# Performance work log

Measured on AMD Instinct MI355X. Metric: run time of the kernel, lower is better.

## Reference

```python
import jax, jax.numpy as jnp
import numpy as np

EPS = 1e-5
DIM = 32          # head_dim
HEADS = 8         # in_channels // dim * heads_ratio = 256 // 32

def hardswish(x):
    return x * jnp.clip(x + 3.0, 0.0, 6.0) / 6.0

def conv1x1(x, w):
    # w: (C_out, C_in); x: (B, C_in, H, W)
    return jnp.einsum('oi,bihw->bohw', w, x)

def dwconv(x, w, pad):
    # depthwise conv, w: (C, 1, kh, kw)
    return jax.lax.conv_general_dilated(
        x, w, (1, 1), [(pad, pad), (pad, pad)],
        dimension_numbers=('NCHW', 'OIHW', 'NCHW'),
        feature_group_count=x.shape[1])

def gconv1x1(x, w, groups):
    # grouped 1x1 conv, w: (C_out, C_in//groups, 1, 1)
    return jax.lax.conv_general_dilated(
        x, w, (1, 1), [(0, 0), (0, 0)],
        dimension_numbers=('NCHW', 'OIHW', 'NCHW'),
        feature_group_count=groups)


def setup_inputs() -> dict:
    key = jax.random.key(0)
    ks = jax.random.split(key, 12)
    B, C, H, W = 16, 256, 32, 32
    td = HEADS * DIM          # 256 (total_dim per branch)
    c3 = 3 * td               # 768
    mid = 4 * C               # 1024 (expand_ratio=4)

    def rn(k, shape, fan_in):
        return jax.random.normal(k, shape, jnp.float32) * (1.0 / np.sqrt(fan_in))

    return {
        'x': jax.random.normal(ks[0], (B, C, H, W), jnp.float32),
        # LiteMLA
        'w_qkv': rn(ks[1], (c3, C), C),                 # 1x1, bias=False, no norm
        'w_agg_dw': rn(ks[2], (c3, 1, 5, 5), 25),       # depthwise 5x5, pad 2
        'w_agg_pw': rn(ks[3], (c3, DIM, 1, 1), DIM),    # grouped 1x1, groups=3*HEADS
        'w_proj': rn(ks[4], (C, 2 * td), 2 * td),       # 1x1, bias=False (BN follows)
        'bn_proj_scale': jnp.ones((C,), jnp.float32) + 0.1 * jax.random.normal(ks[5], (C,), jnp.float32),
        'bn_proj_bias': 0.1 * jax.random.normal(ks[6], (C,), jnp.float32),
        # MBConv
        'w_mb1': rn(ks[7], (mid, C), C),
        'b_mb1': jnp.zeros((mid,), jnp.float32),
        'w_mb_dw': rn(ks[8], (mid, 1, 3, 3), 9),
        'b_mb_dw': jnp.zeros((mid,), jnp.float32),
        'w_mb2': rn(ks[9], (C, mid), mid),              # bias=False (BN follows)
        'bn2_scale': jnp.ones((C,), jnp.float32) + 0.1 * jax.random.normal(ks[10], (C,), jnp.float32),
        'bn2_bias': 0.1 * jax.random.normal(ks[11], (C,), jnp.float32),
    }


def reference(x, w_qkv, w_agg_dw, w_agg_pw, w_proj, bn_proj_scale, bn_proj_bias,
              w_mb1, b_mb1, w_mb_dw, b_mb_dw, w_mb2, bn2_scale, bn2_bias):
    B, C, H, W = x.shape
    # ---- LiteMLA context module (residual) ----
    qkv = conv1x1(x, w_qkv)                                   # (B, 768, H, W)
    agg = gconv1x1(dwconv(qkv, w_agg_dw, 2), w_agg_pw, 3 * HEADS)
    ms = jnp.concatenate([qkv, agg], axis=1)                  # (B, 1536, H, W)
    nh = ms.shape[1] // (3 * DIM)                             # 16 total heads
    t = ms.reshape(B, nh, 3 * DIM, H * W).transpose(0, 1, 3, 2)  # (B, nh, HW, 3*DIM)
    q, k, v = jnp.split(t, 3, axis=-1)                        # each (B, nh, HW, DIM)
    q = jax.nn.relu(q).astype(jnp.float32)
    k = jax.nn.relu(k).astype(jnp.float32)
    v = jnp.pad(v.astype(jnp.float32), ((0, 0), (0, 0), (0, 0), (0, 1)),
                constant_values=1.0)                          # (B, nh, HW, DIM+1)
    kv = jnp.einsum('bhnd,bhne->bhde', k, v)                  # (B, nh, DIM, DIM+1)
    out = jnp.einsum('bhnd,bhde->bhne', q, kv)                # (B, nh, HW, DIM+1)
    out = out[..., :-1] / (out[..., -1:] + EPS)
    out = out.astype(x.dtype)
    out = out.transpose(0, 1, 3, 2).reshape(B, nh * DIM, H, W)  # (B, 512, H, W)
    out = conv1x1(out, w_proj)
    out = out * bn_proj_scale[:, None, None] + bn_proj_bias[:, None, None]
    x = x + out                                               # residual
    # ---- MBConv local module (residual) ----
    h = hardswish(conv1x1(x, w_mb1) + b_mb1[:, None, None])
    h = hardswish(dwconv(h, w_mb_dw, 1) + b_mb_dw[:, None, None])
    h = conv1x1(h, w_mb2)
    h = h * bn2_scale[:, None, None] + bn2_bias[:, None, None]
    return x + h
```

## Files before the change

kernel.cpp:

```cpp
#include <hip/hip_runtime.h>
#include <hip/hip_bf16.h>


typedef unsigned short u16;
typedef __attribute__((ext_vector_type(8))) short short8;
typedef __attribute__((ext_vector_type(4))) short short4v;
typedef __attribute__((ext_vector_type(4))) float f32x4;

#define HW 1024
#define EPSV 1e-5f
#define MFMA16(a, b, c) __builtin_amdgcn_mfma_f32_16x16x32_bf16((a), (b), (c), 0, 0, 0)

__device__ __forceinline__ u16 f2bf(float f) {
    union { __hip_bfloat16 h; u16 u; } c; c.h = __float2bfloat16(f); return c.u;
}
__device__ __forceinline__ float bf2f(u16 u) {
    union { u16 u; __hip_bfloat16 h; } c; c.u = u; return __bfloat162float(c.h);
}
__device__ __forceinline__ float hswish(float v) {
    return v * fminf(fmaxf(v + 3.f, 0.f), 6.f) * (1.f / 6.f);
}

__global__ __launch_bounds__(256) void prep_k(
    const float* __restrict__ x,  u16* __restrict__ xb,
    const float* __restrict__ wq, u16* __restrict__ wqb,
    const float* __restrict__ wp, u16* __restrict__ wpb,
    const float* __restrict__ w1, u16* __restrict__ w1b,
    const float* __restrict__ w2, u16* __restrict__ w2b)
{
    const int N0 = 4194304, N1 = 196608, N2 = 131072, N3 = 262144;
    const int total = N0 + N1 + N2 + N3 + 262144;
    for (int i = blockIdx.x * 256 + threadIdx.x; i < total; i += gridDim.x * 256) {
        int id = i;
        if (id < N0) { xb[id]  = f2bf(x[id]);  continue; } id -= N0;
        if (id < N1) { wqb[id] = f2bf(wq[id]); continue; } id -= N1;
        if (id < N2) { wpb[id] = f2bf(wp[id]); continue; } id -= N2;
        if (id < N3) { w1b[id] = f2bf(w1[id]); continue; } id -= N3;
        w2b[id] = f2bf(w2[id]);
    }
}

template<int EPI>
__global__ __launch_bounds__(256) void gemm_bf(
    const u16* __restrict__ A, const u16* __restrict__ Bact,
    const float* __restrict__ s1, const float* __restrict__ s2,
    const float* __restrict__ Rres, float* __restrict__ outF,
    u16* __restrict__ outB, int M, int K)
{
    const int b  = blockIdx.z;
    const int n0 = blockIdx.x * 128;
    const int m0 = blockIdx.y * 128;
    const int t  = threadIdx.x;
    const int lr = t & 15, lg = (t >> 4) & 3;
    const int wid = t >> 6, wm = wid >> 1, wn = wid & 1;

    __shared__ u16 As[128 * 64];
    __shared__ u16 Bs[128 * 64];

    const u16* Bp = Bact + (size_t)b * K * HW;

    f32x4 zero4 = {0.f, 0.f, 0.f, 0.f};
    f32x4 acc[4][4];
    #pragma unroll
    for (int i = 0; i < 4; ++i)
        #pragma unroll
        for (int j = 0; j < 4; ++j) acc[i][j] = zero4;

    for (int k0 = 0; k0 < K; k0 += 64) {
        {
            const u16* Ab = A + (size_t)m0 * K + k0;
            #pragma unroll
            for (int u = 0; u < 4; ++u) {
                int id = t + u * 256;
                int row = id >> 3, c = id & 7;
                short8 v = *(const short8*)(Ab + (size_t)row * K + c * 8);
                *(short8*)(&As[row * 64 + ((c ^ (row & 7)) * 8)]) = v;
            }
        }
        {
            const u16* Bb = Bp + (size_t)k0 * HW + n0;
            int n = t & 127, kh = t >> 7;
            #pragma unroll
            for (int u = 0; u < 4; ++u) {
                int c = kh * 4 + u;
                short8 v;
                #pragma unroll
                for (int g = 0; g < 8; ++g)
                    v[g] = (short)Bb[(size_t)(c * 8 + g) * HW + n];
                *(short8*)(&Bs[n * 64 + ((c ^ (n & 7)) * 8)]) = v;
            }
        }
        __syncthreads();
        #pragma unroll
        for (int kk = 0; kk < 2; ++kk) {
            short8 a[4], bb[4];
            #pragma unroll
            for (int i = 0; i < 4; ++i) {
                int row = wm * 64 + i * 16 + lr;
                a[i] = *(const short8*)(&As[row * 64 + (((kk * 4 + lg) ^ (lr & 7)) * 8)]);
            }
            #pragma unroll
            for (int j = 0; j < 4; ++j) {
                int row = wn * 64 + j * 16 + lr;
                bb[j] = *(const short8*)(&Bs[row * 64 + (((kk * 4 + lg) ^ (lr & 7)) * 8)]);
            }
            #pragma unroll
            for (int i = 0; i < 4; ++i)
                #pragma unroll
                for (int j = 0; j < 4; ++j)
                    acc[i][j] = MFMA16(a[i], bb[j], acc[i][j]);
        }
        __syncthreads();
    }

    const size_t obase = (size_t)b * M * HW;
    #pragma unroll
    for (int i = 0; i < 4; ++i) {
        #pragma unroll
        for (int r = 0; r < 4; ++r) {
            const int grow = m0 + wm * 64 + i * 16 + lg * 4 + r;
            float p1 = 0.f, p2 = 0.f;
            if (EPI == 1) { p1 = s1[grow]; }
            if (EPI >= 2) { p1 = s1[grow]; p2 = s2[grow]; }
            #pragma unroll
            for (int j = 0; j < 4; ++j) {
                const int gcol = n0 + wn * 64 + j * 16 + lr;
                const size_t off = obase + (size_t)grow * HW + gcol;
                float v = acc[i][j][r];
                if (EPI == 0) { outB[off] = f2bf(v); }
                if (EPI == 1) { v = hswish(v + p1); outB[off] = f2bf(v); }
                if (EPI == 2) { v = v * p1 + p2 + Rres[off]; outF[off] = v; outB[off] = f2bf(v); }
                if (EPI == 3) { v = v * p1 + p2 + Rres[off]; outF[off] = v; }
            }
        }
    }
}

template<int KS, int PAD, int NCH, bool HS>
__global__ __launch_bounds__(256) void dwconv_k(
    const u16* __restrict__ in, const float* __restrict__ w,
    const float* __restrict__ bias, u16* __restrict__ out)
{
    constexpr int T = 32 + 2 * PAD;
    __shared__ float tile[T * T];
    const int plane = blockIdx.x;
    const int c = plane % NCH;
    const u16* ip = in + (size_t)plane * HW;
    const int t = threadIdx.x;
    for (int idx = t; idx < T * T; idx += 256) {
        int r = idx / T, cc = idx % T;
        int gr = r - PAD, gc = cc - PAD;
        float v = 0.f;
        if ((unsigned)gr < 32u && (unsigned)gc < 32u) v = bf2f(ip[gr * 32 + gc]);
        tile[idx] = v;
    }
    float wl[KS * KS];
    #pragma unroll
    for (int u = 0; u < KS * KS; ++u) wl[u] = w[c * KS * KS + u];
    const float bv = HS ? bias[c] : 0.f;
    __syncthreads();
    #pragma unroll
    for (int pj = 0; pj < 4; ++pj) {
        const int px = t + pj * 256;
        const int pr = px >> 5, pc = px & 31;
        float s = bv;
        #pragma unroll
        for (int dr = 0; dr < KS; ++dr)
            #pragma unroll
            for (int dc = 0; dc < KS; ++dc)
                s += tile[(pr + dr) * T + pc + dc] * wl[dr * KS + dc];
        if (HS) s = hswish(s);
        out[(size_t)plane * HW + px] = f2bf(s);
    }
}

__global__ __launch_bounds__(256) void gconv_k(
    const u16* __restrict__ dw, const float* __restrict__ wpw,
    u16* __restrict__ agg)
{
    const int gx = blockIdx.x;
    const int g = gx >> 2, nt = gx & 3;
    const int b = blockIdx.y;
    const int n0 = nt * 256;
    const int t = threadIdx.x;
    __shared__ float dt[32][256];
    __shared__ float wl[32 * 32];
    const u16* dp = dw + ((size_t)b * 768 + g * 32) * HW + n0;
    for (int idx = t; idx < 32 * 256; idx += 256) {
        int i = idx >> 8, nn = idx & 255;
        dt[i][nn] = bf2f(dp[(size_t)i * HW + nn]);
    }
    for (int idx = t; idx < 1024; idx += 256) wl[idx] = wpw[g * 1024 + idx];
    __syncthreads();
    float acc[32] = {};
    #pragma unroll
    for (int i = 0; i < 32; ++i) {
        const float d = dt[i][t];
        #pragma unroll
        for (int oc = 0; oc < 32; ++oc) acc[oc] += wl[oc * 32 + i] * d;
    }
    u16* ap = agg + ((size_t)b * 768 + g * 32) * HW + n0;
    #pragma unroll
    for (int oc = 0; oc < 32; ++oc) ap[(size_t)oc * HW + t] = f2bf(acc[oc]);
}

__global__ __launch_bounds__(64) void kv_k(
    const u16* __restrict__ qkvb, const u16* __restrict__ aggb,
    float* __restrict__ kvp)
{
    const int blk = blockIdx.x;
    const int bh = blk >> 2, nc = blk & 3;
    const int b = bh >> 4, h = bh & 15;
    const u16* src = (h < 8) ? qkvb + ((size_t)b * 768 + h * 96) * HW
                             : aggb + ((size_t)b * 768 + (h - 8) * 96) * HW;
    const u16* kp = src + 32 * HW + nc * 256;
    const u16* vp = src + 64 * HW + nc * 256;
    const int l = threadIdx.x;
    const int lr = l & 15, lg = l >> 4;

    f32x4 zero4 = {0.f, 0.f, 0.f, 0.f};
    f32x4 acc[2][3];
    #pragma unroll
    for (int i = 0; i < 2; ++i)
        #pragma unroll
        for (int j = 0; j < 3; ++j) acc[i][j] = zero4;

    short8 bones;
    #pragma unroll
    for (int g = 0; g < 8; ++g) bones[g] = (lr == 0) ? (short)0x3F80 : (short)0;

    for (int ks = 0; ks < 8; ++ks) {
        const int kn = ks * 32 + lg * 8;
        short8 a0 = *(const short8*)(kp + (size_t)lr * HW + kn);
        short8 a1 = *(const short8*)(kp + (size_t)(16 + lr) * HW + kn);
        #pragma unroll
        for (int g = 0; g < 8; ++g) {
            if (((u16)a0[g]) & 0x8000) a0[g] = 0;
            if (((u16)a1[g]) & 0x8000) a1[g] = 0;
        }
        short8 b0 = *(const short8*)(vp + (size_t)lr * HW + kn);
        short8 b1 = *(const short8*)(vp + (size_t)(16 + lr) * HW + kn);
        acc[0][0] = MFMA16(a0, b0, acc[0][0]);
        acc[0][1] = MFMA16(a0, b1, acc[0][1]);
        acc[0][2] = MFMA16(a0, bones, acc[0][2]);
        acc[1][0] = MFMA16(a1, b0, acc[1][0]);
        acc[1][1] = MFMA16(a1, b1, acc[1][1]);
        acc[1][2] = MFMA16(a1, bones, acc[1][2]);
    }
    float* dst = kvp + (size_t)blk * 1056;
    #pragma unroll
    for (int dt = 0; dt < 2; ++dt)
        #pragma unroll
        for (int et = 0; et < 3; ++et)
            #pragma unroll
            for (int r = 0; r < 4; ++r) {
                const int d = dt * 16 + lg * 4 + r;
                const int e = et * 16 + lr;
                if (et < 2 || lr == 0) dst[d * 33 + e] = acc[dt][et][r];
            }
}

__global__ __launch_bounds__(256) void attn_k(
    const u16* __restrict__ qkvb, const u16* __restrict__ aggb,
    const float* __restrict__ kvp, u16* __restrict__ attnb)
{
    const int blk = blockIdx.x;
    const int bh = blk >> 2, nc = blk & 3;
    const int b = bh >> 4, h = bh & 15;
    const u16* qp = (h < 8) ? qkvb + ((size_t)b * 768 + h * 96) * HW
                            : aggb + ((size_t)b * 768 + (h - 8) * 96) * HW;
    __shared__ u16 qs[256 * 40];
    const int t = threadIdx.x;
    #pragma unroll 4
    for (int u = 0; u < 32; ++u) {
        int id = t + u * 256;
        int d = id >> 8, n = id & 255;
        u16 q = qp[(size_t)d * HW + nc * 256 + n];
        if (q & 0x8000) q = 0;
        qs[n * 40 + d] = q;
    }
    const int lr = t & 15, lg = (t >> 4) & 3, w = t >> 6;

    short8 bf[3];
    const float* kb = kvp + (size_t)bh * 4 * 1056;
    #pragma unroll
    for (int et = 0; et < 3; ++et)
        #pragma unroll
        for (int j = 0; j < 8; ++j) {
            const int d = lg * 8 + j, e = et * 16 + lr;
            float s = 0.f;
            if (e <= 32) {
                #pragma unroll
                for (int c = 0; c < 4; ++c) s += kb[c * 1056 + d * 33 + e];
            }
            bf[et][j] = (short)f2bf(s);
        }
    __syncthreads();

    f32x4 zero4 = {0.f, 0.f, 0.f, 0.f};
    f32x4 acc[4][3];
    #pragma unroll
    for (int i = 0; i < 4; ++i) {
        const int row = w * 64 + i * 16 + lr;
        short8 a = *(const short8*)(&qs[row * 40 + lg * 8]);
        #pragma unroll
        for (int et = 0; et < 3; ++et) acc[i][et] = MFMA16(a, bf[et], zero4);
    }

    u16* ap = attnb + (size_t)b * 512 * HW + (size_t)h * 32 * HW;
    #pragma unroll
    for (int i = 0; i < 4; ++i) {
        float inv[4];
        #pragma unroll
        for (int r = 0; r < 4; ++r) {
            const float den = __shfl(acc[i][2][r], t & 48, 64);
            inv[r] = 1.f / (den + EPSV);
        }
        const int nbase = nc * 256 + w * 64 + i * 16 + lg * 4;
        #pragma unroll
        for (int et = 0; et < 2; ++et) {
            const int e = et * 16 + lr;
            short4v o;
            #pragma unroll
            for (int r = 0; r < 4; ++r) o[r] = (short)f2bf(acc[i][et][r] * inv[r]);
            *(short4v*)(ap + (size_t)e * HW + nbase) = o;
        }
    }
}

extern "C" void kernel_launch(void* const* d_in, const int* in_sizes, int n_in,
                              void* d_out, int out_size, void* d_ws, size_t ws_size,
                              hipStream_t stream)
{
    const float* x        = (const float*)d_in[0];
    const float* w_qkv    = (const float*)d_in[1];
    const float* w_agg_dw = (const float*)d_in[2];
    const float* w_agg_pw = (const float*)d_in[3];
    const float* w_proj   = (const float*)d_in[4];
    const float* bnp_s    = (const float*)d_in[5];
    const float* bnp_b    = (const float*)d_in[6];
    const float* w_mb1    = (const float*)d_in[7];
    const float* b_mb1    = (const float*)d_in[8];
    const float* w_mb_dw  = (const float*)d_in[9];
    const float* b_mb_dw  = (const float*)d_in[10];
    const float* w_mb2    = (const float*)d_in[11];
    const float* bn2_s    = (const float*)d_in[12];
    const float* bn2_b    = (const float*)d_in[13];
    float* out = (float*)d_out;
    char*  W   = (char*)d_ws;

    u16*   qkvb  = (u16*)(W + 0);
    u16*   xb    = (u16*)(W + 25165824);
    u16*   dwb   = (u16*)(W + 33554432);
    u16*   aggb  = (u16*)(W + 58720256);
    float* kvp   = (float*)(W + 83886080);
    u16*   attnb = (u16*)(W + 33554432);
    u16*   h1b   = (u16*)(W + 0);
    u16*   h2b   = (u16*)(W + 58720256);
    float* y1f   = (float*)(W + 92274688);
    u16*   y1b   = (u16*)(W + 109051904);
    u16*   wqb   = (u16*)(W + 117440512);
    u16*   wpb   = (u16*)(W + 117833728);
    u16*   w1b   = (u16*)(W + 118095872);
    u16*   w2b   = (u16*)(W + 118620160);

    prep_k<<<2048, 256, 0, stream>>>(x, xb, w_qkv, wqb, w_proj, wpb,
                                     w_mb1, w1b, w_mb2, w2b);
    gemm_bf<0><<<dim3(8, 6, 16), 256, 0, stream>>>(
        wqb, xb, nullptr, nullptr, nullptr, nullptr, qkvb, 768, 256);
    dwconv_k<5, 2, 768, false><<<dim3(16 * 768), 256, 0, stream>>>(
        qkvb, w_agg_dw, nullptr, dwb);
    gconv_k<<<dim3(96, 16), 256, 0, stream>>>(dwb, w_agg_pw, aggb);
    kv_k<<<dim3(1024), 64, 0, stream>>>(qkvb, aggb, kvp);
    attn_k<<<dim3(1024), 256, 0, stream>>>(qkvb, aggb, kvp, attnb);
    gemm_bf<2><<<dim3(8, 2, 16), 256, 0, stream>>>(
        wpb, attnb, bnp_s, bnp_b, x, y1f, y1b, 256, 512);
    gemm_bf<1><<<dim3(8, 8, 16), 256, 0, stream>>>(
        w1b, y1b, b_mb1, nullptr, nullptr, nullptr, h1b, 1024, 256);
    dwconv_k<3, 1, 1024, true><<<dim3(16 * 1024), 256, 0, stream>>>(
        h1b, w_mb_dw, b_mb_dw, h2b);
    gemm_bf<3><<<dim3(8, 2, 16), 256, 0, stream>>>(
        w2b, h2b, bn2_s, bn2_b, y1f, out, nullptr, 256, 1024);
}
```

Before: 269.3 us.

## Load GEMM tiles directly to LDS and use 64-row tiles for small GEMMs

Result: faster. 261.6 us (-2.9%).

```diff
diff --git a/kernel.cpp b/kernel.cpp
--- a/kernel.cpp
+++ b/kernel.cpp
@@ -19,6 +19,11 @@
 }
 __device__ __forceinline__ float hswish(float v) {
     return v * fminf(fmaxf(v + 3.f, 0.f), 6.f) * (1.f / 6.f);
+}
+__device__ __forceinline__ void gload_lds16(const u16* g, u16* lds) {
+    __builtin_amdgcn_global_load_lds(
+        (const __attribute__((address_space(1))) void*)g,
+        (__attribute__((address_space(3))) void*)lds, 16, 0, 0);
 }
 
 __global__ __launch_bounds__(256) void prep_k(
@@ -40,24 +45,28 @@
     }
 }
 
-template<int EPI>
-__global__ __launch_bounds__(256) void gemm_bf(
+template<int EPI, int TM>
+__global__ __launch_bounds__(TM * 2) void gemm_bf(
     const u16* __restrict__ A, const u16* __restrict__ Bact,
     const float* __restrict__ s1, const float* __restrict__ s2,
     const float* __restrict__ Rres, float* __restrict__ outF,
     u16* __restrict__ outB, int M, int K)
 {
+    constexpr int NW = TM / 32;
     const int b  = blockIdx.z;
     const int n0 = blockIdx.x * 128;
-    const int m0 = blockIdx.y * 128;
+    const int m0 = blockIdx.y * TM;
     const int t  = threadIdx.x;
+    const int l  = t & 63, w = t >> 6;
     const int lr = t & 15, lg = (t >> 4) & 3;
-    const int wid = t >> 6, wm = wid >> 1, wn = wid & 1;
-
-    __shared__ u16 As[128 * 64];
-    __shared__ u16 Bs[128 * 64];
-
-    const u16* Bp = Bact + (size_t)b * K * HW;
+    const int wm = (TM == 128) ? (w >> 1) : 0;
+    const int wn = (TM == 128) ? (w & 1) : w;
+
+    __shared__ __attribute__((aligned(16))) u16 As[TM * 64];
+    __shared__ __attribute__((aligned(16))) u16 Bs[64 * 128];
+
+    const u16* Ab0 = A + (size_t)m0 * K;
+    const u16* Bp  = Bact + (size_t)b * K * HW + n0;
 
     f32x4 zero4 = {0.f, 0.f, 0.f, 0.f};
     f32x4 acc[4][4];
@@ -67,28 +76,21 @@
         for (int j = 0; j < 4; ++j) acc[i][j] = zero4;
 
     for (int k0 = 0; k0 < K; k0 += 64) {
-        {
-            const u16* Ab = A + (size_t)m0 * K + k0;
-            #pragma unroll
-            for (int u = 0; u < 4; ++u) {
-                int id = t + u * 256;
-                int row = id >> 3, c = id & 7;
-                short8 v = *(const short8*)(Ab + (size_t)row * K + c * 8);
-                *(short8*)(&As[row * 64 + ((c ^ (row & 7)) * 8)]) = v;
-            }
-        }
-        {
-            const u16* Bb = Bp + (size_t)k0 * HW + n0;
-            int n = t & 127, kh = t >> 7;
-            #pragma unroll
-            for (int u = 0; u < 4; ++u) {
-                int c = kh * 4 + u;
-                short8 v;
-                #pragma unroll
-                for (int g = 0; g < 8; ++g)
-                    v[g] = (short)Bb[(size_t)(c * 8 + g) * HW + n];
-                *(short8*)(&Bs[n * 64 + ((c ^ (n & 7)) * 8)]) = v;
-            }
+        #pragma unroll
+        for (int u = 0; u < 4; ++u) {
+            int g = (u * NW + w) * 64 + l;
+            int row = g >> 3, cl = g & 7;
+            int cs = cl ^ (row & 7);
+            gload_lds16(Ab0 + (size_t)row * K + k0 + cs * 8,
+                        As + (size_t)(u * NW + w) * 512);
+        }
+        #pragma unroll
+        for (int u = 0; u < 16 / NW; ++u) {
+            int g = (u * NW + w) * 64 + l;
+            int k = g >> 4, cl = g & 15;
+            int cs = cl ^ ((k >> 3) & 7);
+            gload_lds16(Bp + (size_t)(k0 + k) * HW + cs * 8,
+                        Bs + (size_t)(u * NW + w) * 512);
         }
         __syncthreads();
         #pragma unroll
@@ -101,8 +103,13 @@
             }
             #pragma unroll
             for (int j = 0; j < 4; ++j) {
-                int row = wn * 64 + j * 16 + lr;
-                bb[j] = *(const short8*)(&Bs[row * 64 + (((kk * 4 + lg) ^ (lr & 7)) * 8)]);
+                int n = wn * 64 + j * 16 + lr;
+                int c = (n >> 3) ^ ((kk * 4 + lg) & 7);
+                const u16* bp = &Bs[(kk * 32 + lg * 8) * 128 + c * 8 + (n & 7)];
+                short8 v;
+                #pragma unroll
+                for (int jj = 0; jj < 8; ++jj) v[jj] = (short)bp[(size_t)jj * 128];
+                bb[j] = v;
             }
             #pragma unroll
             for (int i = 0; i < 4; ++i)
@@ -366,19 +373,19 @@
 
     prep_k<<<2048, 256, 0, stream>>>(x, xb, w_qkv, wqb, w_proj, wpb,
                                      w_mb1, w1b, w_mb2, w2b);
-    gemm_bf<0><<<dim3(8, 6, 16), 256, 0, stream>>>(
+    gemm_bf<0, 128><<<dim3(8, 6, 16), 256, 0, stream>>>(
         wqb, xb, nullptr, nullptr, nullptr, nullptr, qkvb, 768, 256);
     dwconv_k<5, 2, 768, false><<<dim3(16 * 768), 256, 0, stream>>>(
         qkvb, w_agg_dw, nullptr, dwb);
     gconv_k<<<dim3(96, 16), 256, 0, stream>>>(dwb, w_agg_pw, aggb);
     kv_k<<<dim3(1024), 64, 0, stream>>>(qkvb, aggb, kvp);
     attn_k<<<dim3(1024), 256, 0, stream>>>(qkvb, aggb, kvp, attnb);
-    gemm_bf<2><<<dim3(8, 2, 16), 256, 0, stream>>>(
+    gemm_bf<2, 64><<<dim3(8, 4, 16), 128, 0, stream>>>(
         wpb, attnb, bnp_s, bnp_b, x, y1f, y1b, 256, 512);
-    gemm_bf<1><<<dim3(8, 8, 16), 256, 0, stream>>>(
+    gemm_bf<1, 128><<<dim3(8, 8, 16), 256, 0, stream>>>(
         w1b, y1b, b_mb1, nullptr, nullptr, nullptr, h1b, 1024, 256);
     dwconv_k<3, 1, 1024, true><<<dim3(16 * 1024), 256, 0, stream>>>(
         h1b, w_mb_dw, b_mb_dw, h2b);
-    gemm_bf<3><<<dim3(8, 2, 16), 256, 0, stream>>>(
+    gemm_bf<3, 64><<<dim3(8, 4, 16), 128, 0, stream>>>(
         w2b, h2b, bn2_s, bn2_b, y1f, out, nullptr, 256, 1024);
 }
```
